# Optimization experiments

Hardware: AMD Instinct MI355X
Metric: run time of the kernel (lower is better)

Reference implementation:

```python
import jax, jax.numpy as jnp
import numpy as np

B, N, D, C = 2, 65536, 128, 128          # batch, n_entries, input_dim, channel_dim
DEG, N_ACTIVE, STRIDE = 16, 4096, 16     # ring-neighbor sparse structure


def _build_indices():
    """Replicates the original module's Python intersection loops exactly,
    flattening them into (src_i, src_j, pair_out) gather/scatter index arrays.
    k[:, e, :] = sum_m a[:, i_th[m], :] * b[:, j_th[m], :] for each write slot e.
    Each slot e is written exactly once, so scatter-add == the original set."""
    neigh = [[] for _ in range(N)]
    for t in range(N_ACTIVE):
        i = t * STRIDE
        neigh[i] = [((t + dlt) % N_ACTIVE) * STRIDE for dlt in range(1, DEG + 1)]
    src_i, src_j, out = [], [], []
    e = 0
    for i in range(N):
        if not neigh[i]:
            continue
        i_element = list(neigh[i]) + [i]
        i_set = set(i_element)
        for j in neigh[i]:
            j_list = neigh[j]
            j_set = set(j_list)
            j_th = [m for m in j_list if m in i_set]      # order of j's list
            i_th = [m for m in i_element if m in j_set]   # order of i_element
            for ai, bi in zip(i_th, j_th):
                src_i.append(ai)
                src_j.append(bi)
                out.append(e)
            e += 1
    return (np.asarray(src_i, np.int32), np.asarray(src_j, np.int32),
            np.asarray(out, np.int32))


def setup_inputs() -> dict:
    key = jax.random.key(0)
    ks = jax.random.split(key, 8)
    s = 1.0 / np.sqrt(D)
    src_i, src_j, pair_out = _build_indices()
    return {
        "x": jax.random.normal(ks[0], (B, N, D), jnp.float32),
        "ln_in_w": jnp.ones((D,), jnp.float32),
        "ln_in_b": jnp.zeros((D,), jnp.float32),
        "Wla": jax.random.normal(ks[1], (C, D), jnp.float32) * s,
        "bla": jnp.zeros((C,), jnp.float32),
        "Wga": jax.random.normal(ks[2], (C, D), jnp.float32) * s,
        "bga": jnp.zeros((C,), jnp.float32),
        "Wlb": jax.random.normal(ks[3], (C, D), jnp.float32) * s,
        "blb": jnp.zeros((C,), jnp.float32),
        "Wgb": jax.random.normal(ks[4], (C, D), jnp.float32) * s,
        "bgb": jnp.zeros((C,), jnp.float32),
        "ln_o_w": jnp.ones((C,), jnp.float32),
        "ln_o_b": jnp.zeros((C,), jnp.float32),
        "Wgo": jax.random.normal(ks[5], (D, D), jnp.float32) * s,
        "bgo": jnp.zeros((D,), jnp.float32),
        "Wlo": jax.random.normal(ks[6], (D, C), jnp.float32) * s,
        "blo": jnp.zeros((D,), jnp.float32),
        "src_i": jnp.asarray(src_i),
        "src_j": jnp.asarray(src_j),
        "pair_out": jnp.asarray(pair_out),
    }


def _layernorm(x, w, b, eps=1e-5):
    mu = jnp.mean(x, axis=-1, keepdims=True)
    var = jnp.mean(jnp.square(x - mu), axis=-1, keepdims=True)
    return (x - mu) * jax.lax.rsqrt(var + eps) * w + b


def reference(x, ln_in_w, ln_in_b, Wla, bla, Wga, bga, Wlb, blb, Wgb, bgb,
              ln_o_w, ln_o_b, Wgo, bgo, Wlo, blo, src_i, src_j, pair_out):
    xn = _layernorm(x, ln_in_w, ln_in_b)                              # [B,N,D]
    a = jax.nn.sigmoid(xn @ Wga.T + bga) * (xn @ Wla.T + bla)         # [B,N,C]
    b = jax.nn.sigmoid(xn @ Wgb.T + bgb) * (xn @ Wlb.T + blb)         # [B,N,C]
    # triangular update: gather-multiply-sum-scatter over precomputed pairs
    prod = a[:, src_i, :] * b[:, src_j, :]                            # [B,P,C]
    k = jnp.zeros_like(a).at[:, pair_out, :].add(prod)                # [B,N,C]
    out = jax.nn.sigmoid(xn @ Wgo.T + bgo) * (_layernorm(k, ln_o_w, ln_o_b) @ Wlo.T + blo)
    return out
```

## Files before the change

kernel.cpp:

```cpp
#include <hip/hip_runtime.h>


#define BB 2
#define NN 65536
#define DD 128
#define CC 128
#define NA 4096
#define STR 16
#define WSZ 16384

typedef short short4v __attribute__((ext_vector_type(4)));
typedef short short8v __attribute__((ext_vector_type(8)));
typedef __bf16 bf16x8 __attribute__((ext_vector_type(8)));
typedef float f32x4 __attribute__((ext_vector_type(4)));
typedef float f32x2 __attribute__((ext_vector_type(2)));

__device__ __forceinline__ float sigf(float v) { return 1.0f / (1.0f + __expf(-v)); }
__device__ __forceinline__ short f2bf(float f) {
    union { float f; unsigned u; } v; v.f = f;
    unsigned r = (v.u + 0x7FFFu + ((v.u >> 16) & 1u)) >> 16;
    return (short)r;
}
__device__ __forceinline__ float bf2f(short b) {
    union { unsigned u; float f; } v; v.u = ((unsigned)(unsigned short)b) << 16;
    return v.f;
}
__device__ __forceinline__ bf16x8 s2b(short8v s) {
    union { short8v s; bf16x8 b; } u; u.s = s; return u.b;
}

__global__ __launch_bounds__(256)
void kern_wcvt(const float* __restrict__ Wla, const float* __restrict__ Wga,
               const float* __restrict__ Wlb, const float* __restrict__ Wgb,
               const float* __restrict__ Wgo, const float* __restrict__ Wlo,
               short* __restrict__ wbf)
{
    const int i  = blockIdx.x * 256 + threadIdx.x;
    const int ch = i >> 7, d = i & 127;
    const int pos = ((ch >> 4) * 4 + (d >> 5)) * 512
                  + ((((d >> 3) & 3) * 16 + (ch & 15)) * 8) + (d & 7);
    wbf[pos]           = f2bf(Wla[i]);
    wbf[WSZ + pos]     = f2bf(Wga[i]);
    wbf[2 * WSZ + pos] = f2bf(Wlb[i]);
    wbf[3 * WSZ + pos] = f2bf(Wgb[i]);
    wbf[4 * WSZ + pos] = f2bf(Wgo[i]);
    wbf[5 * WSZ + pos] = f2bf(Wlo[i]);
}

__global__ __launch_bounds__(64)
void kern_ab(const float* __restrict__ x,
             const float* __restrict__ lnw, const float* __restrict__ lnb,
             const short* __restrict__ wbf,
             const float* __restrict__ bla, const float* __restrict__ bga,
             const float* __restrict__ blb, const float* __restrict__ bgb,
             float* __restrict__ cbuf)
{
    const int l     = threadIdx.x;
    const int bid   = blockIdx.x;
    const int batch = bid >> 9;
    const int t0    = ((bid & 511) >> 1) << 4;
    const int nt0   = (bid & 1) * 4;
    const int lr    = l & 15;
    const int q     = l >> 4;
    const int fl    = l * 8;

    const float* xr = x + ((size_t)batch * NN + (size_t)(t0 + lr) * STR) * DD + q * 8;
    f32x4 v[4][2];
    #pragma unroll
    for (int kk = 0; kk < 4; ++kk) {
        v[kk][0] = *(const f32x4*)(xr + kk * 32);
        v[kk][1] = *(const f32x4*)(xr + kk * 32 + 4);
    }
    float s = 0.f, ss = 0.f;
    #pragma unroll
    for (int kk = 0; kk < 4; ++kk)
        #pragma unroll
        for (int h = 0; h < 2; ++h)
            #pragma unroll
            for (int j = 0; j < 4; ++j) { const float f = v[kk][h][j]; s += f; ss += f * f; }
    s += __shfl_xor(s, 16); ss += __shfl_xor(ss, 16);
    s += __shfl_xor(s, 32); ss += __shfl_xor(ss, 32);
    const float mu = s * (1.0f / 128.0f);
    const float rs = rsqrtf(ss * (1.0f / 128.0f) - mu * mu + 1e-5f);

    bf16x8 af[4];
    #pragma unroll
    for (int kk = 0; kk < 4; ++kk) {
        const f32x4 w0 = *(const f32x4*)(lnw + kk * 32 + q * 8);
        const f32x4 w1 = *(const f32x4*)(lnw + kk * 32 + q * 8 + 4);
        const f32x4 b0 = *(const f32x4*)(lnb + kk * 32 + q * 8);
        const f32x4 b1 = *(const f32x4*)(lnb + kk * 32 + q * 8 + 4);
        short8v t;
        #pragma unroll
        for (int j = 0; j < 4; ++j) {
            t[j]     = f2bf((v[kk][0][j] - mu) * rs * w0[j] + b0[j]);
            t[4 + j] = f2bf((v[kk][1][j] - mu) * rs * w1[j] + b1[j]);
        }
        af[kk] = s2b(t);
    }

    const short* wla = wbf;
    const short* wga = wbf + WSZ;
    const short* wlb = wbf + 2 * WSZ;
    const short* wgb = wbf + 3 * WSZ;

    #pragma unroll
    for (int nt = 0; nt < 4; ++nt) {
        const int col  = (nt0 + nt) * 16 + lr;
        const int base = ((nt0 + nt) * 4) * 512 + fl;
        f32x4 ala = {0.f,0.f,0.f,0.f}, aga = {0.f,0.f,0.f,0.f};
        f32x4 alb = {0.f,0.f,0.f,0.f}, agb = {0.f,0.f,0.f,0.f};
        #pragma unroll
        for (int kk = 0; kk < 4; ++kk) {
            const int o = base + kk * 512;
            ala = __builtin_amdgcn_mfma_f32_16x16x32_bf16(af[kk], *(const bf16x8*)(wla + o), ala, 0, 0, 0);
            aga = __builtin_amdgcn_mfma_f32_16x16x32_bf16(af[kk], *(const bf16x8*)(wga + o), aga, 0, 0, 0);
            alb = __builtin_amdgcn_mfma_f32_16x16x32_bf16(af[kk], *(const bf16x8*)(wlb + o), alb, 0, 0, 0);
            agb = __builtin_amdgcn_mfma_f32_16x16x32_bf16(af[kk], *(const bf16x8*)(wgb + o), agb, 0, 0, 0);
        }
        const float xla = bla[col], xga = bga[col], xlb = blb[col], xgb = bgb[col];
        #pragma unroll
        for (int r = 0; r < 4; ++r) {
            const float av = sigf(aga[r] + xga) * (ala[r] + xla);
            const float bv = sigf(agb[r] + xgb) * (alb[r] + xlb);
            cbuf[((size_t)batch * NA + t0 + q * 4 + r) * CC + col] = av * bv;
        }
    }
}

__global__ __launch_bounds__(256)
void kern_out(const float* __restrict__ x,
              const float* __restrict__ lnw,  const float* __restrict__ lnb,
              const float* __restrict__ lnow, const float* __restrict__ lnob,
              const short* __restrict__ wbf,  const float* __restrict__ bgo,
              const float* __restrict__ blo,
              const float* __restrict__ cbuf, float* __restrict__ out)
{
    __shared__ short kls[4][2][16][136];
    const int bid   = blockIdx.x;
    const int swz   = (bid & 7) * 128 + (bid >> 3);
    const int batch = swz >> 9;
    const int ibb   = swz & 511;
    const int row0  = ibb * 128;
    const int t0    = ibb * 8;

    const int tid = threadIdx.x;
    const int wv = tid >> 6, l = tid & 63;
    const int lr = l & 15, lk = l >> 4;
    const int fl = l * 8;

    bf16x8 afx[2][4];
    #pragma unroll
    for (int g = 0; g < 2; ++g) {
        const float* xr = x + ((size_t)batch * NN + row0 + (wv * 2 + g) * 16 + lr) * DD + lk * 8;
        f32x4 v[4][2];
        #pragma unroll
        for (int kk = 0; kk < 4; ++kk) {
            v[kk][0] = *(const f32x4*)(xr + kk * 32);
            v[kk][1] = *(const f32x4*)(xr + kk * 32 + 4);
        }
        float s = 0.f, ss = 0.f;
        #pragma unroll
        for (int kk = 0; kk < 4; ++kk)
            #pragma unroll
            for (int h = 0; h < 2; ++h)
                #pragma unroll
                for (int j = 0; j < 4; ++j) { const float f = v[kk][h][j]; s += f; ss += f * f; }
        s += __shfl_xor(s, 16); ss += __shfl_xor(ss, 16);
        s += __shfl_xor(s, 32); ss += __shfl_xor(ss, 32);
        const float mu = s * (1.0f / 128.0f);
        const float rs = rsqrtf(ss * (1.0f / 128.0f) - mu * mu + 1e-5f);
        #pragma unroll
        for (int kk = 0; kk < 4; ++kk) {
            const f32x4 w0 = *(const f32x4*)(lnw + kk * 32 + lk * 8);
            const f32x4 w1 = *(const f32x4*)(lnw + kk * 32 + lk * 8 + 4);
            const f32x4 b0 = *(const f32x4*)(lnb + kk * 32 + lk * 8);
            const f32x4 b1 = *(const f32x4*)(lnb + kk * 32 + lk * 8 + 4);
            short8v o;
            #pragma unroll
            for (int j = 0; j < 4; ++j) {
                o[j]     = f2bf((v[kk][0][j] - mu) * rs * w0[j] + b0[j]);
                o[4 + j] = f2bf((v[kk][1][j] - mu) * rs * w1[j] + b1[j]);
            }
            afx[g][kk] = s2b(o);
        }
    }

    {
        const int sg = l >> 5;
        const int c4 = (l & 31) * 4;
        const int t  = t0 + wv * 2 + sg;
        f32x4 cv[15];
        #pragma unroll
        for (int sx = 0; sx < 15; ++sx)
            cv[sx] = *(const f32x4*)(cbuf + ((size_t)batch * NA + ((t + sx + 2) & (NA - 1))) * CC + c4);
        short4v z = {0, 0, 0, 0};
        *(short4v*)&kls[wv][sg][15][c4] = z;
        float s0 = 0.f, s1 = 0.f, s2 = 0.f, s3 = 0.f;
        #pragma unroll
        for (int sx = 14; sx >= 0; --sx) {
            s0 += cv[sx][0]; s1 += cv[sx][1]; s2 += cv[sx][2]; s3 += cv[sx][3];
            short4v o; o[0] = f2bf(s0); o[1] = f2bf(s1); o[2] = f2bf(s2); o[3] = f2bf(s3);
            *(short4v*)&kls[wv][sg][sx][c4] = o;
        }
    }

    bf16x8 afk[2][4];
    #pragma unroll
    for (int g = 0; g < 2; ++g) {
        short8v kraw[4];
        #pragma unroll
        for (int kk = 0; kk < 4; ++kk)
            kraw[kk] = *(const short8v*)&kls[wv][g][lr][kk * 32 + lk * 8];
        float ks = 0.f, kss = 0.f;
        #pragma unroll
        for (int kk = 0; kk < 4; ++kk)
            #pragma unroll
            for (int j = 0; j < 8; ++j) { const float f = bf2f(kraw[kk][j]); ks += f; kss += f * f; }
        ks += __shfl_xor(ks, 16); kss += __shfl_xor(kss, 16);
        ks += __shfl_xor(ks, 32); kss += __shfl_xor(kss, 32);
        const float kmu = ks * (1.0f / 128.0f);
        const float krs = rsqrtf(kss * (1.0f / 128.0f) - kmu * kmu + 1e-5f);
        #pragma unroll
        for (int kk = 0; kk < 4; ++kk) {
            const f32x4 w0 = *(const f32x4*)(lnow + kk * 32 + lk * 8);
            const f32x4 w1 = *(const f32x4*)(lnow + kk * 32 + lk * 8 + 4);
            const f32x4 b0 = *(const f32x4*)(lnob + kk * 32 + lk * 8);
            const f32x4 b1 = *(const f32x4*)(lnob + kk * 32 + lk * 8 + 4);
            short8v o;
            #pragma unroll
            for (int j = 0; j < 4; ++j) {
                o[j]     = f2bf((bf2f(kraw[kk][j])     - kmu) * krs * w0[j] + b0[j]);
                o[4 + j] = f2bf((bf2f(kraw[kk][4 + j]) - kmu) * krs * w1[j] + b1[j]);
            }
            afk[g][kk] = s2b(o);
        }
    }

    const short* wgo = wbf + 4 * WSZ;
    const short* wlo = wbf + 5 * WSZ;
    #pragma unroll
    for (int nt = 0; nt < 8; ++nt) {
        bf16x8 bg_[4], bh_[4];
        #pragma unroll
        for (int kk = 0; kk < 4; ++kk) {
            bg_[kk] = *(const bf16x8*)(wgo + (nt * 4 + kk) * 512 + fl);
            bh_[kk] = *(const bf16x8*)(wlo + (nt * 4 + kk) * 512 + fl);
        }
        f32x4 ag0 = {0.f,0.f,0.f,0.f}, ag1 = {0.f,0.f,0.f,0.f};
        f32x4 ah0 = {0.f,0.f,0.f,0.f}, ah1 = {0.f,0.f,0.f,0.f};
        #pragma unroll
        for (int kk = 0; kk < 4; ++kk) {
            ag0 = __builtin_amdgcn_mfma_f32_16x16x32_bf16(afx[0][kk], bg_[kk], ag0, 0, 0, 0);
            ag1 = __builtin_amdgcn_mfma_f32_16x16x32_bf16(afx[1][kk], bg_[kk], ag1, 0, 0, 0);
            ah0 = __builtin_amdgcn_mfma_f32_16x16x32_bf16(afk[0][kk], bh_[kk], ah0, 0, 0, 0);
            ah1 = __builtin_amdgcn_mfma_f32_16x16x32_bf16(afk[1][kk], bh_[kk], ah1, 0, 0, 0);
        }
        const float bgv = bgo[nt * 16 + lr];
        const float blv = blo[nt * 16 + lr];
        #pragma unroll
        for (int r = 0; r < 4; ++r) {
            const size_t rowa = (size_t)batch * NN + row0 + wv * 32 + lk * 4 + r;
            out[rowa * DD + nt * 16 + lr]        = sigf(ag0[r] + bgv) * (ah0[r] + blv);
            out[(rowa + 16) * DD + nt * 16 + lr] = sigf(ag1[r] + bgv) * (ah1[r] + blv);
        }
    }
}

extern "C" void kernel_launch(void* const* d_in, const int* in_sizes, int n_in,
                              void* d_out, int out_size, void* d_ws, size_t ws_size,
                              hipStream_t stream)
{
    const float* x    = (const float*)d_in[0];
    const float* lnw  = (const float*)d_in[1];
    const float* lnb  = (const float*)d_in[2];
    const float* Wla  = (const float*)d_in[3];
    const float* bla  = (const float*)d_in[4];
    const float* Wga  = (const float*)d_in[5];
    const float* bga  = (const float*)d_in[6];
    const float* Wlb  = (const float*)d_in[7];
    const float* blb  = (const float*)d_in[8];
    const float* Wgb  = (const float*)d_in[9];
    const float* bgb  = (const float*)d_in[10];
    const float* lnow = (const float*)d_in[11];
    const float* lnob = (const float*)d_in[12];
    const float* Wgo  = (const float*)d_in[13];
    const float* bgo  = (const float*)d_in[14];
    const float* Wlo  = (const float*)d_in[15];
    const float* blo  = (const float*)d_in[16];

    float* cbuf = (float*)d_ws;
    short* wbf  = (short*)((char*)d_ws + (size_t)BB * NA * CC * 4);
    float* out  = (float*)d_out;

    hipLaunchKernelGGL(kern_wcvt, dim3(WSZ / 256), dim3(256), 0, stream,
                       Wla, Wga, Wlb, Wgb, Wgo, Wlo, wbf);
    hipLaunchKernelGGL(kern_ab, dim3(BB * 512), dim3(64), 0, stream,
                       x, lnw, lnb, wbf, bla, bga, blb, bgb, cbuf);
    hipLaunchKernelGGL(kern_out, dim3(BB * 512), dim3(256), 0, stream,
                       x, lnw, lnb, lnow, lnob, wbf, bgo, blo, cbuf, out);
}
```

Before: 57.77 us.

## Fold layernorm affine params into weights/biases and shrink kern_out blocks

Folds the layernorm scale into the bf16 weight conversion and the layernorm shift into precomputed per-channel bias tables, so the hot kernels only compute (x-mu)*rs with no per-element gamma/beta loads. Replaces the manual bf16 rounding with a native cast. Splits kern_out into 64-thread blocks covering 32 rows each (4096 blocks) with smaller shared memory. This adds a small setup pass to build the bias table, and the folded weights change where bf16 rounding happens.

```diff
diff --git a/kernel.cpp b/kernel.cpp
--- a/kernel.cpp
+++ b/kernel.cpp
@@ -13,13 +13,10 @@
 typedef short short8v __attribute__((ext_vector_type(8)));
 typedef __bf16 bf16x8 __attribute__((ext_vector_type(8)));
 typedef float f32x4 __attribute__((ext_vector_type(4)));
-typedef float f32x2 __attribute__((ext_vector_type(2)));
 
 __device__ __forceinline__ float sigf(float v) { return 1.0f / (1.0f + __expf(-v)); }
-__device__ __forceinline__ short f2bf(float f) {
-    union { float f; unsigned u; } v; v.f = f;
-    unsigned r = (v.u + 0x7FFFu + ((v.u >> 16) & 1u)) >> 16;
-    return (short)r;
+__device__ __forceinline__ short nbf(float f) {
+    union { __bf16 h; short s; } u; u.h = (__bf16)f; return u.s;
 }
 __device__ __forceinline__ float bf2f(short b) {
     union { unsigned u; float f; } v; v.u = ((unsigned)(unsigned short)b) << 16;
@@ -33,27 +30,48 @@
 void kern_wcvt(const float* __restrict__ Wla, const float* __restrict__ Wga,
                const float* __restrict__ Wlb, const float* __restrict__ Wgb,
                const float* __restrict__ Wgo, const float* __restrict__ Wlo,
-               short* __restrict__ wbf)
+               const float* __restrict__ lnw, const float* __restrict__ lnb,
+               const float* __restrict__ lnow, const float* __restrict__ lnob,
+               const float* __restrict__ bla, const float* __restrict__ bga,
+               const float* __restrict__ blb, const float* __restrict__ bgb,
+               const float* __restrict__ bgo, const float* __restrict__ blo,
+               short* __restrict__ wbf, float* __restrict__ vtab)
 {
-    const int i  = blockIdx.x * 256 + threadIdx.x;
-    const int ch = i >> 7, d = i & 127;
-    const int pos = ((ch >> 4) * 4 + (d >> 5)) * 512
-                  + ((((d >> 3) & 3) * 16 + (ch & 15)) * 8) + (d & 7);
-    wbf[pos]           = f2bf(Wla[i]);
-    wbf[WSZ + pos]     = f2bf(Wga[i]);
-    wbf[2 * WSZ + pos] = f2bf(Wlb[i]);
-    wbf[3 * WSZ + pos] = f2bf(Wgb[i]);
-    wbf[4 * WSZ + pos] = f2bf(Wgo[i]);
-    wbf[5 * WSZ + pos] = f2bf(Wlo[i]);
+    const int b = blockIdx.x;
+    if (b < 64) {
+        const int i  = b * 256 + threadIdx.x;
+        const int ch = i >> 7, d = i & 127;
+        const int pos = ((ch >> 4) * 4 + (d >> 5)) * 512
+                      + ((((d >> 3) & 3) * 16 + (ch & 15)) * 8) + (d & 7);
+        const float wi = lnw[d], wo = lnow[d];
+        wbf[pos]           = nbf(Wla[i] * wi);
+        wbf[WSZ + pos]     = nbf(Wga[i] * wi);
+        wbf[2 * WSZ + pos] = nbf(Wlb[i] * wi);
+        wbf[3 * WSZ + pos] = nbf(Wgb[i] * wi);
+        wbf[4 * WSZ + pos] = nbf(Wgo[i] * wi);
+        wbf[5 * WSZ + pos] = nbf(Wlo[i] * wo);
+    } else {
+        const int t = (b - 64) * 256 + threadIdx.x;
+        const int m = t >> 7, c = t & 127;
+        const float* Wr = (m == 0) ? Wla : (m == 1) ? Wga : (m == 2) ? Wlb
+                        : (m == 3) ? Wgb : (m == 4) ? Wgo : Wlo;
+        const float* bb = (m == 5) ? lnob : lnb;
+        const float* bi = (m == 0) ? bla : (m == 1) ? bga : (m == 2) ? blb
+                        : (m == 3) ? bgb : (m == 4) ? bgo : blo;
+        const float* row = Wr + (size_t)c * DD;
+        float acc = 0.f;
+        for (int d = 0; d < DD; d += 4) {
+            const f32x4 w4 = *(const f32x4*)(row + d);
+            const f32x4 b4 = *(const f32x4*)(bb + d);
+            acc += w4[0]*b4[0] + w4[1]*b4[1] + w4[2]*b4[2] + w4[3]*b4[3];
+        }
+        vtab[m * 128 + c] = acc + bi[c];
+    }
 }
 
 __global__ __launch_bounds__(64)
-void kern_ab(const float* __restrict__ x,
-             const float* __restrict__ lnw, const float* __restrict__ lnb,
-             const short* __restrict__ wbf,
-             const float* __restrict__ bla, const float* __restrict__ bga,
-             const float* __restrict__ blb, const float* __restrict__ bgb,
-             float* __restrict__ cbuf)
+void kern_ab(const float* __restrict__ x, const short* __restrict__ wbf,
+             const float* __restrict__ vtab, float* __restrict__ cbuf)
 {
     const int l     = threadIdx.x;
     const int bid   = blockIdx.x;
@@ -82,19 +100,16 @@
     s += __shfl_xor(s, 32); ss += __shfl_xor(ss, 32);
     const float mu = s * (1.0f / 128.0f);
     const float rs = rsqrtf(ss * (1.0f / 128.0f) - mu * mu + 1e-5f);
+    const float p  = -mu * rs;
 
     bf16x8 af[4];
     #pragma unroll
     for (int kk = 0; kk < 4; ++kk) {
-        const f32x4 w0 = *(const f32x4*)(lnw + kk * 32 + q * 8);
-        const f32x4 w1 = *(const f32x4*)(lnw + kk * 32 + q * 8 + 4);
-        const f32x4 b0 = *(const f32x4*)(lnb + kk * 32 + q * 8);
-        const f32x4 b1 = *(const f32x4*)(lnb + kk * 32 + q * 8 + 4);
         short8v t;
         #pragma unroll
         for (int j = 0; j < 4; ++j) {
-            t[j]     = f2bf((v[kk][0][j] - mu) * rs * w0[j] + b0[j]);
-            t[4 + j] = f2bf((v[kk][1][j] - mu) * rs * w1[j] + b1[j]);
+            t[j]     = nbf(v[kk][0][j] * rs + p);
+            t[4 + j] = nbf(v[kk][1][j] * rs + p);
         }
         af[kk] = s2b(t);
     }
@@ -118,41 +133,38 @@
             alb = __builtin_amdgcn_mfma_f32_16x16x32_bf16(af[kk], *(const bf16x8*)(wlb + o), alb, 0, 0, 0);
             agb = __builtin_amdgcn_mfma_f32_16x16x32_bf16(af[kk], *(const bf16x8*)(wgb + o), agb, 0, 0, 0);
         }
-        const float xla = bla[col], xga = bga[col], xlb = blb[col], xgb = bgb[col];
+        const float vla = vtab[col], vga = vtab[128 + col];
+        const float vlb = vtab[256 + col], vgb = vtab[384 + col];
         #pragma unroll
         for (int r = 0; r < 4; ++r) {
-            const float av = sigf(aga[r] + xga) * (ala[r] + xla);
-            const float bv = sigf(agb[r] + xgb) * (alb[r] + xlb);
+            const float av = sigf(aga[r] + vga) * (ala[r] + vla);
+            const float bv = sigf(agb[r] + vgb) * (alb[r] + vlb);
             cbuf[((size_t)batch * NA + t0 + q * 4 + r) * CC + col] = av * bv;
         }
     }
 }
 
-__global__ __launch_bounds__(256)
-void kern_out(const float* __restrict__ x,
-              const float* __restrict__ lnw,  const float* __restrict__ lnb,
-              const float* __restrict__ lnow, const float* __restrict__ lnob,
-              const short* __restrict__ wbf,  const float* __restrict__ bgo,
-              const float* __restrict__ blo,
-              const float* __restrict__ cbuf, float* __restrict__ out)
+__global__ __launch_bounds__(64)
+void kern_out(const float* __restrict__ x, const short* __restrict__ wbf,
+              const float* __restrict__ vtab, const float* __restrict__ cbuf,
+              float* __restrict__ out)
 {
-    __shared__ short kls[4][2][16][136];
+    __shared__ short kls[2][16][136];
     const int bid   = blockIdx.x;
-    const int swz   = (bid & 7) * 128 + (bid >> 3);
-    const int batch = swz >> 9;
-    const int ibb   = swz & 511;
-    const int row0  = ibb * 128;
-    const int t0    = ibb * 8;
-
-    const int tid = threadIdx.x;
-    const int wv = tid >> 6, l = tid & 63;
+    const int swz   = (bid & 7) * 512 + (bid >> 3);
+    const int batch = swz >> 11;
+    const int ib    = swz & 2047;
+    const int row0  = ib * 32;
+    const int t0    = ib * 2;
+
+    const int l  = threadIdx.x;
     const int lr = l & 15, lk = l >> 4;
     const int fl = l * 8;
 
     bf16x8 afx[2][4];
     #pragma unroll
     for (int g = 0; g < 2; ++g) {
-        const float* xr = x + ((size_t)batch * NN + row0 + (wv * 2 + g) * 16 + lr) * DD + lk * 8;
+        const float* xr = x + ((size_t)batch * NN + row0 + g * 16 + lr) * DD + lk * 8;
         f32x4 v[4][2];
         #pragma unroll
         for (int kk = 0; kk < 4; ++kk) {
@@ -170,17 +182,14 @@
         s += __shfl_xor(s, 32); ss += __shfl_xor(ss, 32);
         const float mu = s * (1.0f / 128.0f);
         const float rs = rsqrtf(ss * (1.0f / 128.0f) - mu * mu + 1e-5f);
-        #pragma unroll
-        for (int kk = 0; kk < 4; ++kk) {
-            const f32x4 w0 = *(const f32x4*)(lnw + kk * 32 + lk * 8);
-            const f32x4 w1 = *(const f32x4*)(lnw + kk * 32 + lk * 8 + 4);
-            const f32x4 b0 = *(const f32x4*)(lnb + kk * 32 + lk * 8);
-            const f32x4 b1 = *(const f32x4*)(lnb + kk * 32 + lk * 8 + 4);
+        const float p  = -mu * rs;
+        #pragma unroll
+        for (int kk = 0; kk < 4; ++kk) {
             short8v o;
             #pragma unroll
             for (int j = 0; j < 4; ++j) {
-                o[j]     = f2bf((v[kk][0][j] - mu) * rs * w0[j] + b0[j]);
-                o[4 + j] = f2bf((v[kk][1][j] - mu) * rs * w1[j] + b1[j]);
+                o[j]     = nbf(v[kk][0][j] * rs + p);
+                o[4 + j] = nbf(v[kk][1][j] * rs + p);
             }
             afx[g][kk] = s2b(o);
         }
@@ -189,19 +198,19 @@
     {
         const int sg = l >> 5;
         const int c4 = (l & 31) * 4;
-        const int t  = t0 + wv * 2 + sg;
+        const int t  = t0 + sg;
         f32x4 cv[15];
         #pragma unroll
         for (int sx = 0; sx < 15; ++sx)
             cv[sx] = *(const f32x4*)(cbuf + ((size_t)batch * NA + ((t + sx + 2) & (NA - 1))) * CC + c4);
         short4v z = {0, 0, 0, 0};
-        *(short4v*)&kls[wv][sg][15][c4] = z;
+        *(short4v*)&kls[sg][15][c4] = z;
         float s0 = 0.f, s1 = 0.f, s2 = 0.f, s3 = 0.f;
         #pragma unroll
         for (int sx = 14; sx >= 0; --sx) {
             s0 += cv[sx][0]; s1 += cv[sx][1]; s2 += cv[sx][2]; s3 += cv[sx][3];
-            short4v o; o[0] = f2bf(s0); o[1] = f2bf(s1); o[2] = f2bf(s2); o[3] = f2bf(s3);
-            *(short4v*)&kls[wv][sg][sx][c4] = o;
+            short4v o; o[0] = nbf(s0); o[1] = nbf(s1); o[2] = nbf(s2); o[3] = nbf(s3);
+            *(short4v*)&kls[sg][sx][c4] = o;
         }
     }
 
@@ -211,7 +220,7 @@
         short8v kraw[4];
         #pragma unroll
         for (int kk = 0; kk < 4; ++kk)
-            kraw[kk] = *(const short8v*)&kls[wv][g][lr][kk * 32 + lk * 8];
+            kraw[kk] = *(const short8v*)&kls[g][lr][kk * 32 + lk * 8];
         float ks = 0.f, kss = 0.f;
         #pragma unroll
         for (int kk = 0; kk < 4; ++kk)
@@ -221,24 +230,21 @@
         ks += __shfl_xor(ks, 32); kss += __shfl_xor(kss, 32);
         const float kmu = ks * (1.0f / 128.0f);
         const float krs = rsqrtf(kss * (1.0f / 128.0f) - kmu * kmu + 1e-5f);
-        #pragma unroll
-        for (int kk = 0; kk < 4; ++kk) {
-            const f32x4 w0 = *(const f32x4*)(lnow + kk * 32 + lk * 8);
-            const f32x4 w1 = *(const f32x4*)(lnow + kk * 32 + lk * 8 + 4);
-            const f32x4 b0 = *(const f32x4*)(lnob + kk * 32 + lk * 8);
-            const f32x4 b1 = *(const f32x4*)(lnob + kk * 32 + lk * 8 + 4);
+        const float kp  = -kmu * krs;
+        #pragma unroll
+        for (int kk = 0; kk < 4; ++kk) {
             short8v o;
             #pragma unroll
-            for (int j = 0; j < 4; ++j) {
-                o[j]     = f2bf((bf2f(kraw[kk][j])     - kmu) * krs * w0[j] + b0[j]);
-                o[4 + j] = f2bf((bf2f(kraw[kk][4 + j]) - kmu) * krs * w1[j] + b1[j]);
-            }
+            for (int j = 0; j < 8; ++j)
+                o[j] = nbf(bf2f(kraw[kk][j]) * krs + kp);
             afk[g][kk] = s2b(o);
         }
     }
 
     const short* wgo = wbf + 4 * WSZ;
     const short* wlo = wbf + 5 * WSZ;
+    const float* vgo = vtab + 4 * 128;
+    const float* vlo = vtab + 5 * 128;
     #pragma unroll
     for (int nt = 0; nt < 8; ++nt) {
         bf16x8 bg_[4], bh_[4];
@@ -256,13 +262,14 @@
             ah0 = __builtin_amdgcn_mfma_f32_16x16x32_bf16(afk[0][kk], bh_[kk], ah0, 0, 0, 0);
             ah1 = __builtin_amdgcn_mfma_f32_16x16x32_bf16(afk[1][kk], bh_[kk], ah1, 0, 0, 0);
         }
-        const float bgv = bgo[nt * 16 + lr];
-        const float blv = blo[nt * 16 + lr];
+        const int   col = nt * 16 + lr;
+        const float vg  = vgo[col];
+        const float vl  = vlo[col];
         #pragma unroll
         for (int r = 0; r < 4; ++r) {
-            const size_t rowa = (size_t)batch * NN + row0 + wv * 32 + lk * 4 + r;
-            out[rowa * DD + nt * 16 + lr]        = sigf(ag0[r] + bgv) * (ah0[r] + blv);
-            out[(rowa + 16) * DD + nt * 16 + lr] = sigf(ag1[r] + bgv) * (ah1[r] + blv);
+            const size_t rowa = (size_t)batch * NN + row0 + lk * 4 + r;
+            out[rowa * DD + col]        = sigf(ag0[r] + vg) * (ah0[r] + vl);
+            out[(rowa + 16) * DD + col] = sigf(ag1[r] + vg) * (ah1[r] + vl);
         }
     }
 }
@@ -291,12 +298,15 @@
 
     float* cbuf = (float*)d_ws;
     short* wbf  = (short*)((char*)d_ws + (size_t)BB * NA * CC * 4);
+    float* vtab = (float*)((char*)wbf + 6 * WSZ * sizeof(short));
     float* out  = (float*)d_out;
 
-    hipLaunchKernelGGL(kern_wcvt, dim3(WSZ / 256), dim3(256), 0, stream,
-                       Wla, Wga, Wlb, Wgb, Wgo, Wlo, wbf);
+    hipLaunchKernelGGL(kern_wcvt, dim3(67), dim3(256), 0, stream,
+                       Wla, Wga, Wlb, Wgb, Wgo, Wlo,
+                       lnw, lnb, lnow, lnob,
+                       bla, bga, blb, bgb, bgo, blo, wbf, vtab);
     hipLaunchKernelGGL(kern_ab, dim3(BB * 512), dim3(64), 0, stream,
-                       x, lnw, lnb, wbf, bla, bga, blb, bgb, cbuf);
-    hipLaunchKernelGGL(kern_out, dim3(BB * 512), dim3(256), 0, stream,
-                       x, lnw, lnb, lnow, lnob, wbf, bgo, blo, cbuf, out);
-}
+                       x, wbf, vtab, cbuf);
+    hipLaunchKernelGGL(kern_out, dim3(BB * 2048), dim3(64), 0, stream,
+                       x, wbf, vtab, cbuf, out);
+}
```

Result: faster. 51.72 us (-10.5%).
